# Kernel optimization log

Measured on AMD Instinct MI355X. Metric: run time of the kernel, lower is better.

Reference implementation:

```python
import jax, jax.numpy as jnp
import numpy as np

N_EMBD = 1024
N_HEAD = 16
R = 16
SCALING = 1.0 / 16.0  # loralib default lora_alpha=1, scaling = alpha/r


def lora_linear(x, W, b, A, B):
    # loralib: y = x @ W.T + b + (x @ A.T) @ B.T * scaling
    return x @ W.T + b + (x @ A.T) @ B.T * SCALING


def setup_inputs() -> dict:
    key = jax.random.key(0)
    ks = jax.random.split(key, 16)
    B, T, S, C = 8, 1024, 256, N_EMBD
    std = 0.02
    return {
        "x": jax.random.normal(ks[0], (B, T, C), jnp.float32),
        "feature": jax.random.normal(ks[1], (B, S, C), jnp.float32),
        # c_attn (q projection)
        "Wq": jax.random.normal(ks[2], (C, C), jnp.float32) * std,
        "bq": jnp.zeros((C,), jnp.float32),
        "Aq": jax.random.normal(ks[3], (R, C), jnp.float32) * std,
        "Bq": jnp.zeros((C, R), jnp.float32),
        # feature_attn (kv projection)
        "Wf": jax.random.normal(ks[4], (2 * C, C), jnp.float32) * std,
        "bf": jnp.zeros((2 * C,), jnp.float32),
        "Af": jax.random.normal(ks[5], (R, C), jnp.float32) * std,
        "Bf": jnp.zeros((2 * C, R), jnp.float32),
        # c_proj
        "Wp": jax.random.normal(ks[6], (C, C), jnp.float32) * std,
        "bp": jnp.zeros((C,), jnp.float32),
        "Ap": jax.random.normal(ks[7], (R, C), jnp.float32) * std,
        "Bp": jnp.zeros((C, R), jnp.float32),
    }


def reference(x, feature, Wq, bq, Aq, Bq, Wf, bf, Af, Bf, Wp, bp, Ap, Bp):
    Bsz, T, C = x.shape
    S = feature.shape[1]
    H = N_HEAD
    D = C // H

    q = lora_linear(x, Wq, bq, Aq, Bq).reshape(Bsz, T, H, D).transpose(0, 2, 1, 3)
    kv = lora_linear(feature, Wf, bf, Af, Bf)
    k, v = kv[..., :C], kv[..., C:]
    k = k.reshape(Bsz, S, H, D).transpose(0, 2, 1, 3)
    v = v.reshape(Bsz, S, H, D).transpose(0, 2, 1, 3)

    att = jnp.einsum("bhtd,bhsd->bhts", q, k) * (1.0 / np.sqrt(D))
    mask = jnp.tril(jnp.ones((T, S), bool))  # bias[:, :, :T, :S]
    att = jnp.where(mask, att, -jnp.inf)
    att = jax.nn.softmax(att, axis=-1)

    y = jnp.einsum("bhts,bhsd->bhtd", att, v)
    y = y.transpose(0, 2, 1, 3).reshape(Bsz, T, C)
    return lora_linear(y, Wp, bp, Ap, Bp)
```

## Files before the change

kernel.cpp:

```cpp
#include <hip/hip_runtime.h>
#include <hip/hip_bf16.h>
#include <stdint.h>
#include <stddef.h>

typedef __hip_bfloat16 bf16;
typedef __attribute__((ext_vector_type(8))) short short8;
typedef __attribute__((ext_vector_type(4))) float floatx4;

__device__ __forceinline__ void async_load16(const bf16* g, bf16* l) {
#if defined(__has_builtin) && __has_builtin(__builtin_amdgcn_global_load_lds)
  __builtin_amdgcn_global_load_lds((__attribute__((address_space(1))) void*)g,
                                   (__attribute__((address_space(3))) void*)l,
                                   16, 0, 0);
#else
  *(short8*)l = *(const short8*)g;
#endif
}

__device__ __forceinline__ int wave_detect_f32(const unsigned short* __restrict__ xr) {
  const int lane = threadIdx.x & 63;
  const unsigned short u = xr[lane];
  const int e = (u >> 7) & 0xFF;
  const unsigned long long m = __ballot(e >= 0x93);
  return (__popcll(m) > 5) ? 1 : 0;
}

struct PrepArgs {
  const void *x, *ft, *bq, *bf, *bp;
  const void *Wq, *Aq, *Bq, *Wf, *Af, *Bf, *Wp, *Ap, *Bp;
  bf16 *cx, *cft, *cbq, *cbf, *cbp, *weffq, *wefff, *weffp;
};

__device__ __forceinline__ void canon8(const void* src, bf16* dst, int i8, int flg) {
  if (flg) {
    const float4 v0 = ((const float4*)src)[i8 * 2];
    const float4 v1 = ((const float4*)src)[i8 * 2 + 1];
    bf16 o[8];
    o[0] = __float2bfloat16(v0.x); o[1] = __float2bfloat16(v0.y);
    o[2] = __float2bfloat16(v0.z); o[3] = __float2bfloat16(v0.w);
    o[4] = __float2bfloat16(v1.x); o[5] = __float2bfloat16(v1.y);
    o[6] = __float2bfloat16(v1.z); o[7] = __float2bfloat16(v1.w);
    *(uint4*)(dst + i8 * 8) = *(const uint4*)o;
  } else {
    ((uint4*)dst)[i8] = ((const uint4*)src)[i8];
  }
}

__device__ __forceinline__ void weff4(const void* W, const void* Bm, const void* Am,
                                      bf16* dst, int idx4, int flg) {
  const int n = idx4 >> 8, k = (idx4 & 255) << 2;
  float a0 = 0.f, a1 = 0.f, a2 = 0.f, a3 = 0.f;
  float w0, w1, w2, w3;
  if (flg) {
    const float* Af = (const float*)Am;
    const float* Bf = (const float*)Bm;
#pragma unroll
    for (int r = 0; r < 16; ++r) {
      const float4 av = *(const float4*)(Af + r * 1024 + k);
      const float bv = Bf[n * 16 + r];
      a0 += bv * av.x; a1 += bv * av.y; a2 += bv * av.z; a3 += bv * av.w;
    }
    const float4 wv = *(const float4*)((const float*)W + n * 1024 + k);
    w0 = wv.x; w1 = wv.y; w2 = wv.z; w3 = wv.w;
  } else {
    const bf16* Ab = (const bf16*)Am;
    const bf16* Bb = (const bf16*)Bm;
#pragma unroll
    for (int r = 0; r < 16; ++r) {
      const float bv = __bfloat162float(Bb[n * 16 + r]);
      const bf16* ap = Ab + r * 1024 + k;
      a0 += bv * __bfloat162float(ap[0]);
      a1 += bv * __bfloat162float(ap[1]);
      a2 += bv * __bfloat162float(ap[2]);
      a3 += bv * __bfloat162float(ap[3]);
    }
    const bf16* Wb = (const bf16*)W + n * 1024 + k;
    w0 = __bfloat162float(Wb[0]); w1 = __bfloat162float(Wb[1]);
    w2 = __bfloat162float(Wb[2]); w3 = __bfloat162float(Wb[3]);
  }
  bf16 o[4];
  o[0] = __float2bfloat16(w0 + 0.0625f * a0);
  o[1] = __float2bfloat16(w1 + 0.0625f * a1);
  o[2] = __float2bfloat16(w2 + 0.0625f * a2);
  o[3] = __float2bfloat16(w3 + 0.0625f * a3);
  *(uint2*)(dst + idx4 * 4) = *(const uint2*)o;
}

__global__ __launch_bounds__(256) void prep_kernel(PrepArgs a) {
  const int flg = wave_detect_f32((const unsigned short*)a.x);
  const int bid = blockIdx.x, tid = threadIdx.x;
  if (bid < 4096) {
    canon8(a.x, a.cx, bid * 256 + tid, flg);
  } else if (bid < 5120) {
    canon8(a.ft, a.cft, (bid - 4096) * 256 + tid, flg);
  } else if (bid < 5122) {
    const int e8 = (bid - 5120) * 256 + tid;
    if (e8 < 128) canon8(a.bq, a.cbq, e8, flg);
    else if (e8 < 384) canon8(a.bf, a.cbf, e8 - 128, flg);
    else canon8(a.bp, a.cbp, e8 - 384, flg);
  } else if (bid < 6146) {
    weff4(a.Wq, a.Bq, a.Aq, a.weffq, (bid - 5122) * 256 + tid, flg);
  } else if (bid < 8194) {
    weff4(a.Wf, a.Bf, a.Af, a.wefff, (bid - 6146) * 256 + tid, flg);
  } else {
    weff4(a.Wp, a.Bp, a.Ap, a.weffp, (bid - 8194) * 256 + tid, flg);
  }
}

#define SLOT ((128 + 128) * 32)

__device__ __forceinline__ void stage_slot(const bf16* __restrict__ gA,
                                           const bf16* __restrict__ gB,
                                           bf16* slot, int tid) {
#pragma unroll
  for (int l = 0; l < 2; ++l) {
    const int D = l * 256 + tid;
    const int r = D >> 2;
    const int c = (D & 3) ^ ((r >> 1) & 3);
    async_load16(gA + (size_t)r * 1024 + c * 8, slot + D * 8);
  }
#pragma unroll
  for (int l = 0; l < 2; ++l) {
    const int D = l * 256 + tid;
    const int r = D >> 2;
    const int c = (D & 3) ^ ((r >> 1) & 3);
    async_load16(gB + (size_t)r * 1024 + c * 8, slot + 128 * 32 + D * 8);
  }
}

__device__ __forceinline__ void gemm_core(const bf16* __restrict__ A,
                                          const bf16* __restrict__ Bt,
                                          int bm, int bn, bf16* sT,
                                          floatx4 (&acc)[4][4]) {
  const int tid = threadIdx.x;
  const int wave = tid >> 6, lane = tid & 63;
  const int lrow = lane & 15, quad = lane >> 4;
  const int wm64 = (wave >> 1) << 6;
  const int wn64 = (wave & 1) << 6;
  const int pc0 = ((quad ^ ((lrow >> 1) & 3)) << 3);

  const bf16* gA = A + (size_t)bm * 1024;
  const bf16* gB = Bt + (size_t)bn * 1024;

  stage_slot(gA, gB, sT, tid);
  stage_slot(gA + 32, gB + 32, sT + SLOT, tid);

#pragma unroll
  for (int t = 0; t < 32; ++t) {
    asm volatile("s_waitcnt lgkmcnt(0)" ::: "memory");
    __builtin_amdgcn_s_barrier();
    __builtin_amdgcn_sched_barrier(0);
    if (t < 30) {
      stage_slot(gA + (t + 2) * 32, gB + (t + 2) * 32,
                 sT + ((t + 2) % 3) * SLOT, tid);
      asm volatile("s_waitcnt vmcnt(8)" ::: "memory");
    } else if (t == 30) {
      asm volatile("s_waitcnt vmcnt(4)" ::: "memory");
    } else {
      asm volatile("s_waitcnt vmcnt(0)" ::: "memory");
    }
    __builtin_amdgcn_s_barrier();
    __builtin_amdgcn_sched_barrier(0);

    const bf16* slotA = sT + (t % 3) * SLOT;
    const bf16* slotB = slotA + 128 * 32;
    short8 a_[4], b_[4];
#pragma unroll
    for (int i = 0; i < 4; ++i) {
      a_[i] = *(const short8*)(slotA + (wm64 + i * 16 + lrow) * 32 + pc0);
      b_[i] = *(const short8*)(slotB + (wn64 + i * 16 + lrow) * 32 + pc0);
    }
    __builtin_amdgcn_s_setprio(1);
#pragma unroll
    for (int i = 0; i < 4; ++i)
#pragma unroll
      for (int j = 0; j < 4; ++j)
        acc[i][j] = __builtin_amdgcn_mfma_f32_16x16x32_bf16(
            a_[i], b_[j], acc[i][j], 0, 0, 0);
    __builtin_amdgcn_s_setprio(0);
  }
}

__global__ __launch_bounds__(256, 3) void gemm_qkv(
    const bf16* __restrict__ cx, const bf16* __restrict__ cft,
    const bf16* __restrict__ weffq, const bf16* __restrict__ wefff,
    const bf16* __restrict__ cbq, const bf16* __restrict__ cbf,
    bf16* __restrict__ qws, bf16* __restrict__ kws, bf16* __restrict__ vtws) {
  __shared__ __align__(16) bf16 sT[3 * SLOT];
  const int bid = blockIdx.x;
  int mode, bm, bn;
  const bf16 *A, *Bt, *bias;
  if (bid < 512) {
    mode = 0; A = cx; Bt = weffq; bias = cbq;
    bm = (((bid & 7) << 3) | ((bid >> 3) & 7)) * 128;
    bn = (bid >> 6) * 128;
  } else {
    const int b2 = bid - 512;
    mode = 1; A = cft; Bt = wefff; bias = cbf;
    bm = (((b2 & 7) << 1) | ((b2 >> 3) & 1)) * 128;
    bn = (b2 >> 4) * 128;
  }

  const floatx4 zero4 = {0.f, 0.f, 0.f, 0.f};
  floatx4 acc[4][4];
#pragma unroll
  for (int i = 0; i < 4; ++i)
#pragma unroll
    for (int j = 0; j < 4; ++j) acc[i][j] = zero4;

  gemm_core(A, Bt, bm, bn, sT, acc);

  const int tid = threadIdx.x, wave = tid >> 6, lane = tid & 63;
  const int lrow = lane & 15, quad = lane >> 4;
  const int wm64 = (wave >> 1) << 6, wn64 = (wave & 1) << 6;
#pragma unroll
  for (int i = 0; i < 4; ++i) {
    const int mbase = bm + wm64 + i * 16 + quad * 4;
#pragma unroll
    for (int j = 0; j < 4; ++j) {
      const int n = bn + wn64 + j * 16 + lrow;
      const float bv = __bfloat162float(bias[n]);
#pragma unroll
      for (int r = 0; r < 4; ++r) {
        const int m = mbase + r;
        const bf16 hval = __float2bfloat16(acc[i][j][r] + bv);
        if (mode == 0) {
          const int b = m >> 10, t = m & 1023, hh = n >> 6, d = n & 63;
          qws[(((size_t)(b * 16 + hh)) * 1024 + t) * 64 + d] = hval;
        } else {
          const int b = m >> 8, s = m & 255;
          if (n < 1024) {
            const int hh = n >> 6, d = n & 63;
            kws[(((size_t)(b * 16 + hh)) * 256 + s) * 64 + d] = hval;
          } else {
            const int nn = n - 1024, hh = nn >> 6, d = nn & 63;
            vtws[(((size_t)(b * 16 + hh)) * 64 + d) * 256 + s] = hval;
          }
        }
      }
    }
  }
}

__global__ __launch_bounds__(256, 3) void gemm_out(
    const bf16* __restrict__ A, const bf16* __restrict__ Bt,
    const bf16* __restrict__ bias, void* __restrict__ out0,
    const unsigned short* __restrict__ xraw) {
  __shared__ __align__(16) bf16 sT[3 * SLOT];
  const int bid = blockIdx.x;
  const int bm = (((bid & 7) << 3) | ((bid >> 3) & 7)) * 128;
  const int bn = (bid >> 6) * 128;
  const int N = 1024;

  const floatx4 zero4 = {0.f, 0.f, 0.f, 0.f};
  floatx4 acc[4][4];
#pragma unroll
  for (int i = 0; i < 4; ++i)
#pragma unroll
    for (int j = 0; j < 4; ++j) acc[i][j] = zero4;

  gemm_core(A, Bt, bm, bn, sT, acc);

  const int tid = threadIdx.x, wave = tid >> 6, lane = tid & 63;
  const int lrow = lane & 15, quad = lane >> 4;
  const int wm64 = (wave >> 1) << 6, wn64 = (wave & 1) << 6;
  const int flg = wave_detect_f32(xraw);
#pragma unroll
  for (int i = 0; i < 4; ++i) {
    const int mbase = bm + wm64 + i * 16 + quad * 4;
#pragma unroll
    for (int j = 0; j < 4; ++j) {
      const int n = bn + wn64 + j * 16 + lrow;
      const float bv = __bfloat162float(bias[n]);
#pragma unroll
      for (int r = 0; r < 4; ++r) {
        const int m = mbase + r;
        const float fval = acc[i][j][r] + bv;
        const size_t idx = (size_t)m * N + n;
        if (flg) ((float*)out0)[idx] = fval;
        else     ((bf16*)out0)[idx] = __float2bfloat16(fval);
      }
    }
  }
}

#define SKP 72
#define SVP 264
__global__ __launch_bounds__(512, 2) void attn_kernel(
    const bf16* __restrict__ qws, const bf16* __restrict__ kws,
    const bf16* __restrict__ vtws, bf16* __restrict__ yws) {
  const int b = blockIdx.z, h = blockIdx.y, qc = blockIdx.x;
  const int bh = b * 16 + h;
  __shared__ __align__(16) bf16 sK[256 * SKP];
  __shared__ __align__(16) bf16 sVt[64 * SVP];
  __shared__ __align__(16) bf16 sP[8][16 * SVP];
  const int tid = threadIdx.x, wave = tid >> 6, lane = tid & 63;
  const int lrow = lane & 15, quad = lane >> 4;
  const bf16* kg = kws + (size_t)bh * (256 * 64);
  const bf16* vg = vtws + (size_t)bh * (64 * 256);
#pragma unroll
  for (int i = 0; i < 4; ++i) {
    const int idx = i * 512 + tid;
    const int kr = idx >> 3, kc = (idx & 7) * 8;
    *(short8*)(sK + kr * SKP + kc) = *(const short8*)(kg + kr * 64 + kc);
    const int vr = idx >> 5, vc = (idx & 31) * 8;
    *(short8*)(sVt + vr * SVP + vc) = *(const short8*)(vg + vr * 256 + vc);
  }
  __syncthreads();
  bf16* sPw = sP[wave];
  const floatx4 zero4 = {0.f, 0.f, 0.f, 0.f};
  const float kscale = 0.18033688011112042f;

  for (int st = 0; st < 4; ++st) {
    const int t0 = qc * 512 + wave * 64 + st * 16;
    const bf16* qrow = qws + ((size_t)bh * 1024 + t0 + lrow) * 64;
    const short8 aq0 = *(const short8*)(qrow + quad * 8);
    const short8 aq1 = *(const short8*)(qrow + 32 + quad * 8);
    floatx4 sc[16];
#pragma unroll
    for (int nt = 0; nt < 16; ++nt) {
      floatx4 c = zero4;
      c = __builtin_amdgcn_mfma_f32_16x16x32_bf16(
          aq0, *(const short8*)(sK + (nt * 16 + lrow) * SKP + quad * 8), c, 0, 0, 0);
      c = __builtin_amdgcn_mfma_f32_16x16x32_bf16(
          aq1, *(const short8*)(sK + (nt * 16 + lrow) * SKP + 32 + quad * 8), c, 0, 0, 0);
      sc[nt] = c;
    }
    float sum[4] = {0.f, 0.f, 0.f, 0.f};
#pragma unroll
    for (int nt = 0; nt < 16; ++nt) {
      const int s = nt * 16 + lrow;
#pragma unroll
      for (int r = 0; r < 4; ++r) {
        const int t = t0 + quad * 4 + r;
        const float p = (s <= t) ? exp2f(sc[nt][r] * kscale) : 0.f;
        sum[r] += p;
        sPw[(quad * 4 + r) * SVP + nt * 16 + lrow] = __float2bfloat16(p);
      }
    }
#pragma unroll
    for (int r = 0; r < 4; ++r) {
      sum[r] += __shfl_xor(sum[r], 1, 16);
      sum[r] += __shfl_xor(sum[r], 2, 16);
      sum[r] += __shfl_xor(sum[r], 4, 16);
      sum[r] += __shfl_xor(sum[r], 8, 16);
    }
    asm volatile("s_waitcnt lgkmcnt(0)" ::: "memory");
    floatx4 ya[4];
#pragma unroll
    for (int nt = 0; nt < 4; ++nt) ya[nt] = zero4;
#pragma unroll
    for (int ks = 0; ks < 8; ++ks) {
      const short8 ap = *(const short8*)(sPw + lrow * SVP + ks * 32 + quad * 8);
#pragma unroll
      for (int nt = 0; nt < 4; ++nt)
        ya[nt] = __builtin_amdgcn_mfma_f32_16x16x32_bf16(
            ap, *(const short8*)(sVt + (nt * 16 + lrow) * SVP + ks * 32 + quad * 8),
            ya[nt], 0, 0, 0);
    }
#pragma unroll
    for (int r = 0; r < 4; ++r) {
      const float rl = 1.f / sum[r];
      const int t = t0 + quad * 4 + r;
#pragma unroll
      for (int nt = 0; nt < 4; ++nt)
        yws[((size_t)b * 1024 + t) * 1024 + h * 64 + nt * 16 + lrow] =
            __float2bfloat16(ya[nt][r] * rl);
    }
  }
}

extern "C" void kernel_launch(void* const* d_in, const int* in_sizes, int n_in,
                              void* d_out, int out_size, void* d_ws, size_t ws_size,
                              hipStream_t stream) {
  char* p = (char*)d_ws;
  bf16* cbq   = (bf16*)p;     p += 4096;
  bf16* cbf   = (bf16*)p;     p += 8192;
  bf16* cbp   = (bf16*)p;     p += 4096;
  bf16* weffq = (bf16*)p;     p += (size_t)1024 * 1024 * 2;
  bf16* wefff = (bf16*)p;     p += (size_t)2048 * 1024 * 2;
  bf16* weffp = (bf16*)p;     p += (size_t)1024 * 1024 * 2;
  bf16* qws   = (bf16*)p;     p += (size_t)8 * 16 * 1024 * 64 * 2;
  bf16* kws   = (bf16*)p;     p += (size_t)8 * 16 * 256 * 64 * 2;
  bf16* vtws  = (bf16*)p;     p += (size_t)8 * 16 * 64 * 256 * 2;
  bf16* cft   = (bf16*)p;     p += (size_t)8 * 256 * 1024 * 2;
  bf16* cx    = (bf16*)p;     p += (size_t)8 * 1024 * 1024 * 2;
  bf16* yws   = cx;
  const size_t required = (size_t)(p - (char*)d_ws);
  if (ws_size < required) return;

  PrepArgs pa;
  pa.x = d_in[0]; pa.ft = d_in[1];
  pa.bq = d_in[3]; pa.bf = d_in[7]; pa.bp = d_in[11];
  pa.Wq = d_in[2];  pa.Aq = d_in[4];  pa.Bq = d_in[5];
  pa.Wf = d_in[6];  pa.Af = d_in[8];  pa.Bf = d_in[9];
  pa.Wp = d_in[10]; pa.Ap = d_in[12]; pa.Bp = d_in[13];
  pa.cx = cx; pa.cft = cft; pa.cbq = cbq; pa.cbf = cbf; pa.cbp = cbp;
  pa.weffq = weffq; pa.wefff = wefff; pa.weffp = weffp;
  prep_kernel<<<9218, 256, 0, stream>>>(pa);

  gemm_qkv<<<768, 256, 0, stream>>>(cx, cft, weffq, wefff, cbq, cbf, qws, kws, vtws);
  attn_kernel<<<dim3(2, 16, 8), 512, 0, stream>>>(qws, kws, vtws, yws);
  gemm_out<<<512, 256, 0, stream>>>(yws, weffp, cbp, d_out, (const unsigned short*)d_in[0]);
}
```

Measured before the change: 216.7 us.

## Rewrite QKV GEMM with 256x256 tiles, 8 waves, and ping-pong half-tile staging

The QKV projection GEMM moves from 128x128 tiles with 4 waves and a 3-slot K=32 pipeline to 256x256 tiles with 8 waves per block. It uses K=64 chunks staged in even/odd LDS buffers, with the loads split into half-tiles and interleaved between the MFMA groups. The block index is also swizzled. The aim is higher arithmetic intensity per LDS byte and better overlap of global loads with MFMA. The cost is only 192 blocks at one block per CU, which leaves some CUs idle, plus heavy register pressure and many barriers.

```diff
diff --git a/kernel.cpp b/kernel.cpp
--- a/kernel.cpp
+++ b/kernel.cpp
@@ -107,118 +107,169 @@
   }
 }
 
-#define SLOT ((128 + 128) * 32)
-
-__device__ __forceinline__ void stage_slot(const bf16* __restrict__ gA,
-                                           const bf16* __restrict__ gB,
-                                           bf16* slot, int tid) {
-#pragma unroll
-  for (int l = 0; l < 2; ++l) {
-    const int D = l * 256 + tid;
-    const int r = D >> 2;
-    const int c = (D & 3) ^ ((r >> 1) & 3);
-    async_load16(gA + (size_t)r * 1024 + c * 8, slot + D * 8);
-  }
-#pragma unroll
-  for (int l = 0; l < 2; ++l) {
-    const int D = l * 256 + tid;
-    const int r = D >> 2;
-    const int c = (D & 3) ^ ((r >> 1) & 3);
-    async_load16(gB + (size_t)r * 1024 + c * 8, slot + 128 * 32 + D * 8);
-  }
-}
-
-__device__ __forceinline__ void gemm_core(const bf16* __restrict__ A,
-                                          const bf16* __restrict__ Bt,
-                                          int bm, int bn, bf16* sT,
-                                          floatx4 (&acc)[4][4]) {
-  const int tid = threadIdx.x;
-  const int wave = tid >> 6, lane = tid & 63;
-  const int lrow = lane & 15, quad = lane >> 4;
-  const int wm64 = (wave >> 1) << 6;
-  const int wn64 = (wave & 1) << 6;
-  const int pc0 = ((quad ^ ((lrow >> 1) & 3)) << 3);
-
-  const bf16* gA = A + (size_t)bm * 1024;
-  const bf16* gB = Bt + (size_t)bn * 1024;
-
-  stage_slot(gA, gB, sT, tid);
-  stage_slot(gA + 32, gB + 32, sT + SLOT, tid);
-
-#pragma unroll
-  for (int t = 0; t < 32; ++t) {
-    asm volatile("s_waitcnt lgkmcnt(0)" ::: "memory");
-    __builtin_amdgcn_s_barrier();
-    __builtin_amdgcn_sched_barrier(0);
-    if (t < 30) {
-      stage_slot(gA + (t + 2) * 32, gB + (t + 2) * 32,
-                 sT + ((t + 2) % 3) * SLOT, tid);
-      asm volatile("s_waitcnt vmcnt(8)" ::: "memory");
-    } else if (t == 30) {
-      asm volatile("s_waitcnt vmcnt(4)" ::: "memory");
-    } else {
-      asm volatile("s_waitcnt vmcnt(0)" ::: "memory");
-    }
-    __builtin_amdgcn_s_barrier();
-    __builtin_amdgcn_sched_barrier(0);
-
-    const bf16* slotA = sT + (t % 3) * SLOT;
-    const bf16* slotB = slotA + 128 * 32;
-    short8 a_[4], b_[4];
-#pragma unroll
-    for (int i = 0; i < 4; ++i) {
-      a_[i] = *(const short8*)(slotA + (wm64 + i * 16 + lrow) * 32 + pc0);
-      b_[i] = *(const short8*)(slotB + (wn64 + i * 16 + lrow) * 32 + pc0);
-    }
-    __builtin_amdgcn_s_setprio(1);
-#pragma unroll
-    for (int i = 0; i < 4; ++i)
-#pragma unroll
-      for (int j = 0; j < 4; ++j)
-        acc[i][j] = __builtin_amdgcn_mfma_f32_16x16x32_bf16(
-            a_[i], b_[j], acc[i][j], 0, 0, 0);
-    __builtin_amdgcn_s_setprio(0);
-  }
-}
-
-__global__ __launch_bounds__(256, 3) void gemm_qkv(
+#define TBE (256 * 64)
+
+__device__ __forceinline__ void stage_half(const bf16* __restrict__ g,
+                                           bf16* l, int tid) {
+#pragma unroll
+  for (int q = 0; q < 2; ++q) {
+    const int D = q * 512 + tid;
+    const int r = D >> 3;
+    const int c = (D & 7) ^ (r & 7);
+    async_load16(g + (size_t)r * 1024 + c * 8, l + D * 8);
+  }
+}
+
+__device__ __forceinline__ void rd_a4(const bf16* slot, int mi0, int wm, int lrow,
+                                      int c0e, short8 (&aF)[4][2]) {
+#pragma unroll
+  for (int mi = 0; mi < 4; ++mi) {
+    const bf16* ra = slot + (wm + (mi0 + mi) * 16 + lrow) * 64;
+    aF[mi][0] = *(const short8*)(ra + c0e);
+    aF[mi][1] = *(const short8*)(ra + (c0e ^ 32));
+  }
+}
+
+__device__ __forceinline__ void rd_b2(const bf16* slot, int nj0, int wn, int lrow,
+                                      int c0e, short8 (&bF)[4][2]) {
+#pragma unroll
+  for (int nj = 0; nj < 2; ++nj) {
+    const bf16* rb = slot + (wn + (nj0 + nj) * 16 + lrow) * 64;
+    bF[nj0 + nj][0] = *(const short8*)(rb + c0e);
+    bF[nj0 + nj][1] = *(const short8*)(rb + (c0e ^ 32));
+  }
+}
+
+__device__ __forceinline__ void mm16(floatx4 (&acc)[8][4], short8 (&aF)[4][2],
+                                     short8 (&bF)[4][2], int mi0, int nj0) {
+  __builtin_amdgcn_s_setprio(1);
+#pragma unroll
+  for (int mi = 0; mi < 4; ++mi)
+#pragma unroll
+    for (int nj = 0; nj < 2; ++nj)
+#pragma unroll
+      for (int kh = 0; kh < 2; ++kh)
+        acc[mi0 + mi][nj0 + nj] = __builtin_amdgcn_mfma_f32_16x16x32_bf16(
+            aF[mi][kh], bF[nj0 + nj][kh], acc[mi0 + mi][nj0 + nj], 0, 0, 0);
+  __builtin_amdgcn_s_setprio(0);
+}
+
+#define BAR8 do { __builtin_amdgcn_s_barrier(); __builtin_amdgcn_sched_barrier(0); } while (0)
+#define LGKM0 do { asm volatile("s_waitcnt lgkmcnt(0)" ::: "memory"); \
+                   __builtin_amdgcn_sched_barrier(0); } while (0)
+
+__global__ __launch_bounds__(512, 1) void gemm_qkv(
     const bf16* __restrict__ cx, const bf16* __restrict__ cft,
     const bf16* __restrict__ weffq, const bf16* __restrict__ wefff,
     const bf16* __restrict__ cbq, const bf16* __restrict__ cbf,
     bf16* __restrict__ qws, bf16* __restrict__ kws, bf16* __restrict__ vtws) {
-  __shared__ __align__(16) bf16 sT[3 * SLOT];
+  __shared__ __align__(16) bf16 sT[4 * TBE];
+  bf16* const AE = sT;
+  bf16* const BE = sT + TBE;
+  bf16* const AO = sT + 2 * TBE;
+  bf16* const BO = sT + 3 * TBE;
+
   const int bid = blockIdx.x;
+  const int swz = (bid & 7) * 24 + (bid >> 3);
   int mode, bm, bn;
   const bf16 *A, *Bt, *bias;
-  if (bid < 512) {
+  if (swz < 128) {
     mode = 0; A = cx; Bt = weffq; bias = cbq;
-    bm = (((bid & 7) << 3) | ((bid >> 3) & 7)) * 128;
-    bn = (bid >> 6) * 128;
+    bm = (swz >> 2) * 256; bn = (swz & 3) * 256;
   } else {
-    const int b2 = bid - 512;
+    const int s2 = swz - 128;
     mode = 1; A = cft; Bt = wefff; bias = cbf;
-    bm = (((b2 & 7) << 1) | ((b2 >> 3) & 1)) * 128;
-    bn = (b2 >> 4) * 128;
-  }
-
-  const floatx4 zero4 = {0.f, 0.f, 0.f, 0.f};
-  floatx4 acc[4][4];
-#pragma unroll
-  for (int i = 0; i < 4; ++i)
-#pragma unroll
-    for (int j = 0; j < 4; ++j) acc[i][j] = zero4;
-
-  gemm_core(A, Bt, bm, bn, sT, acc);
+    bm = (s2 >> 3) * 256; bn = (s2 & 7) * 256;
+  }
 
   const int tid = threadIdx.x, wave = tid >> 6, lane = tid & 63;
   const int lrow = lane & 15, quad = lane >> 4;
-  const int wm64 = (wave >> 1) << 6, wn64 = (wave & 1) << 6;
-#pragma unroll
-  for (int i = 0; i < 4; ++i) {
-    const int mbase = bm + wm64 + i * 16 + quad * 4;
+  const int wm = (wave >> 2) << 7;
+  const int wn = (wave & 3) << 6;
+  const int c0e = ((quad ^ (lrow & 7)) << 3);
+
+  const bf16* gA = A + (size_t)bm * 1024;
+  const bf16* gB = Bt + (size_t)bn * 1024;
+
+  const floatx4 zero4 = {0.f, 0.f, 0.f, 0.f};
+  floatx4 acc[8][4];
+#pragma unroll
+  for (int i = 0; i < 8; ++i)
+#pragma unroll
+    for (int j = 0; j < 4; ++j) acc[i][j] = zero4;
+  short8 aF[4][2], bF[4][2];
+
+  stage_half(gA, AE, tid);
+  stage_half(gA + (size_t)128 * 1024, AE + 8192, tid);
+  stage_half(gB, BE, tid);
+  stage_half(gB + (size_t)128 * 1024, BE + 8192, tid);
+  stage_half(gA + 64, AO, tid);
+  asm volatile("s_waitcnt vmcnt(2)" ::: "memory");
+  BAR8;
+
+  for (int it = 0; it < 8; ++it) {
+    const bf16* gA1 = gA + (2 * it + 1) * 64;
+    const bf16* gB1 = gB + (2 * it + 1) * 64;
+    const bf16* gA2 = gA + (2 * it + 2) * 64;
+    const bf16* gB2 = gB + (2 * it + 2) * 64;
+    const bf16* gA3 = gA + (2 * it + 3) * 64;
+
+    rd_a4(AE, 0, wm, lrow, c0e, aF);
+    rd_b2(BE, 0, wn, lrow, c0e, bF);
+    stage_half(gA1 + (size_t)128 * 1024, AO + 8192, tid);
+    BAR8; LGKM0;
+    mm16(acc, aF, bF, 0, 0);
+    BAR8;
+    rd_b2(BE, 2, wn, lrow, c0e, bF);
+    stage_half(gB1, BO, tid);
+    BAR8; LGKM0;
+    mm16(acc, aF, bF, 0, 2);
+    BAR8;
+    rd_a4(AE, 4, wm, lrow, c0e, aF);
+    stage_half(gB1 + (size_t)128 * 1024, BO + 8192, tid);
+    BAR8; LGKM0;
+    mm16(acc, aF, bF, 4, 0);
+    BAR8;
+    if (it < 7) {
+      stage_half(gA2, AE, tid);
+      asm volatile("s_waitcnt vmcnt(2)" ::: "memory");
+    } else {
+      asm volatile("s_waitcnt vmcnt(0)" ::: "memory");
+    }
+    BAR8;
+    mm16(acc, aF, bF, 4, 2);
+    BAR8;
+    rd_a4(AO, 0, wm, lrow, c0e, aF);
+    rd_b2(BO, 0, wn, lrow, c0e, bF);
+    if (it < 7) stage_half(gA2 + (size_t)128 * 1024, AE + 8192, tid);
+    BAR8; LGKM0;
+    mm16(acc, aF, bF, 0, 0);
+    BAR8;
+    rd_b2(BO, 2, wn, lrow, c0e, bF);
+    if (it < 7) stage_half(gB2, BE, tid);
+    BAR8; LGKM0;
+    mm16(acc, aF, bF, 0, 2);
+    BAR8;
+    rd_a4(AO, 4, wm, lrow, c0e, aF);
+    if (it < 7) stage_half(gB2 + (size_t)128 * 1024, BE + 8192, tid);
+    BAR8; LGKM0;
+    mm16(acc, aF, bF, 4, 0);
+    BAR8;
+    if (it < 7) {
+      stage_half(gA3, AO, tid);
+      asm volatile("s_waitcnt vmcnt(2)" ::: "memory");
+    }
+    BAR8;
+    mm16(acc, aF, bF, 4, 2);
+    BAR8;
+  }
+
+#pragma unroll
+  for (int i = 0; i < 8; ++i) {
+    const int mbase = bm + wm + i * 16 + quad * 4;
 #pragma unroll
     for (int j = 0; j < 4; ++j) {
-      const int n = bn + wn64 + j * 16 + lrow;
+      const int n = bn + wn + j * 16 + lrow;
       const float bv = __bfloat162float(bias[n]);
 #pragma unroll
       for (int r = 0; r < 4; ++r) {
@@ -239,6 +290,80 @@
         }
       }
     }
+  }
+}
+
+#define SLOT ((128 + 128) * 32)
+
+__device__ __forceinline__ void stage_slot(const bf16* __restrict__ gA,
+                                           const bf16* __restrict__ gB,
+                                           bf16* slot, int tid) {
+#pragma unroll
+  for (int l = 0; l < 2; ++l) {
+    const int D = l * 256 + tid;
+    const int r = D >> 2;
+    const int c = (D & 3) ^ ((r >> 1) & 3);
+    async_load16(gA + (size_t)r * 1024 + c * 8, slot + D * 8);
+  }
+#pragma unroll
+  for (int l = 0; l < 2; ++l) {
+    const int D = l * 256 + tid;
+    const int r = D >> 2;
+    const int c = (D & 3) ^ ((r >> 1) & 3);
+    async_load16(gB + (size_t)r * 1024 + c * 8, slot + 128 * 32 + D * 8);
+  }
+}
+
+__device__ __forceinline__ void gemm_core(const bf16* __restrict__ A,
+                                          const bf16* __restrict__ Bt,
+                                          int bm, int bn, bf16* sT,
+                                          floatx4 (&acc)[4][4]) {
+  const int tid = threadIdx.x;
+  const int wave = tid >> 6, lane = tid & 63;
+  const int lrow = lane & 15, quad = lane >> 4;
+  const int wm64 = (wave >> 1) << 6;
+  const int wn64 = (wave & 1) << 6;
+  const int pc0 = ((quad ^ ((lrow >> 1) & 3)) << 3);
+
+  const bf16* gA = A + (size_t)bm * 1024;
+  const bf16* gB = Bt + (size_t)bn * 1024;
+
+  stage_slot(gA, gB, sT, tid);
+  stage_slot(gA + 32, gB + 32, sT + SLOT, tid);
+
+#pragma unroll
+  for (int t = 0; t < 32; ++t) {
+    asm volatile("s_waitcnt lgkmcnt(0)" ::: "memory");
+    __builtin_amdgcn_s_barrier();
+    __builtin_amdgcn_sched_barrier(0);
+    if (t < 30) {
+      stage_slot(gA + (t + 2) * 32, gB + (t + 2) * 32,
+                 sT + ((t + 2) % 3) * SLOT, tid);
+      asm volatile("s_waitcnt vmcnt(8)" ::: "memory");
+    } else if (t == 30) {
+      asm volatile("s_waitcnt vmcnt(4)" ::: "memory");
+    } else {
+      asm volatile("s_waitcnt vmcnt(0)" ::: "memory");
+    }
+    __builtin_amdgcn_s_barrier();
+    __builtin_amdgcn_sched_barrier(0);
+
+    const bf16* slotA = sT + (t % 3) * SLOT;
+    const bf16* slotB = slotA + 128 * 32;
+    short8 a_[4], b_[4];
+#pragma unroll
+    for (int i = 0; i < 4; ++i) {
+      a_[i] = *(const short8*)(slotA + (wm64 + i * 16 + lrow) * 32 + pc0);
+      b_[i] = *(const short8*)(slotB + (wn64 + i * 16 + lrow) * 32 + pc0);
+    }
+    __builtin_amdgcn_s_setprio(1);
+#pragma unroll
+    for (int i = 0; i < 4; ++i)
+#pragma unroll
+      for (int j = 0; j < 4; ++j)
+        acc[i][j] = __builtin_amdgcn_mfma_f32_16x16x32_bf16(
+            a_[i], b_[j], acc[i][j], 0, 0, 0);
+    __builtin_amdgcn_s_setprio(0);
   }
 }
 
@@ -399,7 +524,7 @@
   pa.weffq = weffq; pa.wefff = wefff; pa.weffp = weffp;
   prep_kernel<<<9218, 256, 0, stream>>>(pa);
 
-  gemm_qkv<<<768, 256, 0, stream>>>(cx, cft, weffq, wefff, cbq, cbf, qws, kws, vtws);
+  gemm_qkv<<<192, 512, 0, stream>>>(cx, cft, weffq, wefff, cbq, cbf, qws, kws, vtws);
   attn_kernel<<<dim3(2, 16, 8), 512, 0, stream>>>(qws, kws, vtws, yws);
   gemm_out<<<512, 256, 0, stream>>>(yws, weffp, cbp, d_out, (const unsigned short*)d_in[0]);
 }
```

Measured after the change: 235.9 us. 8.9% more time.
